# Optimization experiments

Measured on AMD Instinct MI355X. Metric: run time of the kernel, lower is better.

## Reference

```python
import jax, jax.numpy as jnp
import numpy as np

B, N, C_IN, C_EMB, G = 16, 1024, 16, 64, 128
NEG = -1e12


def _lap(m):
    # m @ D^-1/2, transpose, @ D^-1/2  (matches torch code incl. transpose)
    d = jnp.sum(m, axis=1) ** -0.5
    return (m * d[None, :]).T * d[None, :]


def setup_inputs():
    key = jax.random.key(0)
    ks = jax.random.split(key, 16)
    f = jax.random.normal
    return {
        'x': f(ks[0], (B, C_IN, N), jnp.float32),
        'ct': f(ks[1], (B, C_EMB, N), jnp.float32),
        'graph_data': jax.random.uniform(ks[2], (2, N, N), dtype=jnp.float32),
        'emb_w': f(ks[3], (C_EMB, C_IN)) / np.sqrt(C_IN).astype(np.float32),
        'emb_b': f(ks[4], (C_EMB,)) * 0.01,
        'emb2_w': f(ks[5], (N, N)) / np.sqrt(N).astype(np.float32),
        'emb2_b': f(ks[6], (N,)) * 0.01,
        'att_W': f(ks[7], (C_EMB, C_EMB)) / np.sqrt(C_EMB).astype(np.float32),
        'att_a': f(ks[8], (2 * C_EMB, 1)) / np.sqrt(2 * C_EMB).astype(np.float32),
        'att_GL': f(ks[9], (N, G)) / np.sqrt(G).astype(np.float32),
        'uai_w': f(ks[10], (C_EMB, C_EMB)) / np.sqrt(C_EMB).astype(np.float32),
        'uai_b': f(ks[11], (C_EMB,)) * 0.01,
        'lin1_w': f(ks[12], (C_EMB, C_EMB)) / np.sqrt(C_EMB).astype(np.float32),
        'lin2_w': f(ks[13], (C_EMB, C_EMB)) / np.sqrt(C_EMB).astype(np.float32),
        'lin2_b': f(ks[14], (C_EMB,)) * 0.01,
        'ln_w': jnp.ones((C_EMB, N), jnp.float32),
        'ln_b': jnp.zeros((C_EMB, N), jnp.float32),
    }


def reference(x, ct, graph_data, emb_w, emb_b, emb2_w, emb2_b, att_W, att_a,
              att_GL, uai_w, uai_b, lin1_w, lin2_w, lin2_b, ln_w, ln_b):
    # emb: Conv1d k=1 -> leaky_relu -> Linear over node axis N
    h0 = jax.nn.leaky_relu(jnp.einsum('bcn,ec->ben', x, emb_w) + emb_b[None, :, None])
    h0 = jnp.einsum('ben,mn->bem', h0, emb2_w) + emb2_b[None, None, :]
    inp = jnp.swapaxes(h0, 1, 2)  # [B,N,C']

    # InterpositionAttention (repeat/cat factorized: e_ij = leakyrelu(a1.h_i + a2.h_j))
    eye = jnp.eye(N, dtype=x.dtype)
    adj_att = jax.nn.softmax(jax.nn.relu(att_GL @ att_GL.T), axis=-1) + eye
    h = inp @ att_W  # [B,N,C']
    e = jax.nn.leaky_relu((h @ att_a[:C_EMB]) + jnp.swapaxes(h @ att_a[C_EMB:], 1, 2))  # [B,N,N]
    att = jax.nn.softmax(jnp.where(adj_att > 0, e, NEG), axis=2)
    x_att = jnp.swapaxes(jax.nn.relu(att @ h), 1, 2)  # [B,C',N]

    # UAI module (eval mode: dropout off -> all MC samples equal -> sigma = 0)
    mu = jnp.swapaxes(x_att, 1, 2) @ uai_w.T + uai_b  # [B,N,C']
    x_uai = jnp.swapaxes(mu, 1, 2)  # [B,C',N]

    g1 = _lap(graph_data[0] + eye)
    g2 = _lap(graph_data[1] + eye)

    # learned adjacency from pairwise squared distances (cdist p=2, squared)
    xf = jnp.swapaxes(x_uai, 1, 2)  # [B,N,C']
    sq = jnp.sum(xf * xf, axis=-1)
    d2 = jnp.maximum(sq[:, :, None] + sq[:, None, :] - 2.0 * (xf @ jnp.swapaxes(xf, 1, 2)), 0.0)
    gl = jax.nn.softmax(jnp.exp(-d2 / (2.0 * C_EMB)) + eye, axis=-1)  # sigma^2 = emb_size

    def ln(z):  # LayerNorm over last two dims [C', N]
        m = jnp.mean(z, axis=(1, 2), keepdims=True)
        v = jnp.var(z, axis=(1, 2), keepdims=True)
        return (z - m) / jnp.sqrt(v + 1e-5) * ln_w + ln_b

    l1 = lambda z: jnp.einsum('oc,bcn->bon', lin1_w, z)
    l2 = lambda z: jnp.einsum('oc,bcn->bon', lin2_w, z) + lin2_b[None, :, None]

    x_new = ln(l1(x_uai) @ gl + l1(l1(x_uai) @ g1) @ g2)
    ft = jax.nn.gelu(ln(l2(x_uai) @ gl + l2(l2(x_uai) @ g1) @ g2), approximate=False)
    rt = ft  # rt is computed by the identical expression (dropout off)

    ct_new = ft * ct + x_new - ft * x_new
    ht = rt * jax.nn.elu(ct_new) + x_uai - rt * x_uai
    return (ht, ct_new)
```

## Files before the change

### kernel.cpp

```cpp
#include <hip/hip_runtime.h>
#include <math.h>

typedef unsigned short u16;
typedef __attribute__((ext_vector_type(8))) short short8;
typedef __attribute__((ext_vector_type(4))) float floatx4;

constexpr int BATCH = 16;
constexpr int NI = 1024;
constexpr int CE = 64;
constexpr int CI = 16;
constexpr long long NN2  = (long long)NI * NI;
constexpr long long BCN  = (long long)BATCH * CE * NI;
constexpr long long BNv  = (long long)BATCH * NI;
constexpr long long BNN  = (long long)BATCH * NI * NI;
constexpr long long S1 = (long long)CE * NI;
constexpr long long S2 = 2 * S1;
constexpr int ZERON = (int)(2 * BNv + 80);

__device__ __forceinline__ float lrelu01(float x) { return x > 0.f ? x : 0.01f * x; }

__device__ __forceinline__ u16 f2bf(float f) {
  unsigned u = __builtin_bit_cast(unsigned, f);
  return (u16)((u + 0x7fffu + ((u >> 16) & 1u)) >> 16);
}
__device__ __forceinline__ float bf2f(u16 h) {
  unsigned u = ((unsigned)h) << 16;
  return __builtin_bit_cast(float, u);
}
__device__ __forceinline__ unsigned fkey(float f) {
  unsigned u = __builtin_bit_cast(unsigned, f);
  return (u & 0x80000000u) ? ~u : (u | 0x80000000u);
}
__device__ __forceinline__ float funkey(unsigned k) {
  unsigned u = (k & 0x80000000u) ? (k & 0x7fffffffu) : ~k;
  return __builtin_bit_cast(float, u);
}

__device__ __forceinline__ void gload16(const u16* g, u16* l) {
  __builtin_amdgcn_global_load_lds(
      (const __attribute__((address_space(1))) void*)g,
      (__attribute__((address_space(3))) void*)l, 16, 0, 0);
}

__device__ __forceinline__ void fence13() {
  __builtin_amdgcn_sched_barrier(0);
  asm volatile("s_waitcnt vmcnt(2) lgkmcnt(0)" ::: "memory");
  __builtin_amdgcn_s_barrier();
  __builtin_amdgcn_sched_barrier(0);
}

template<int N>
__device__ __forceinline__ void fence_bar() {
  __builtin_amdgcn_sched_barrier(0);
  if constexpr (N == 0) asm volatile("s_waitcnt vmcnt(0)" ::: "memory");
  else if constexpr (N == 1) asm volatile("s_waitcnt vmcnt(1)" ::: "memory");
  else if constexpr (N == 2) asm volatile("s_waitcnt vmcnt(2)" ::: "memory");
  else if constexpr (N == 3) asm volatile("s_waitcnt vmcnt(3)" ::: "memory");
  else if constexpr (N == 4) asm volatile("s_waitcnt vmcnt(4)" ::: "memory");
  else if constexpr (N == 6) asm volatile("s_waitcnt vmcnt(6)" ::: "memory");
  else asm volatile("s_waitcnt vmcnt(0)" ::: "memory");
  __builtin_amdgcn_s_barrier();
  __builtin_amdgcn_sched_barrier(0);
}

template<int BM, int BN, int MODE>
__global__ __launch_bounds__(256) void mgemm(
    const u16* __restrict__ Ag, const u16* __restrict__ B1g, const u16* __restrict__ B2g,
    int K1, int K, int lda, int ldb, long long bsA, long long bsB1,
    float* __restrict__ Cf, u16* __restrict__ Cb, int ldc, long long bsC,
    const float* __restrict__ aux1, const float* __restrict__ aux2,
    const float* __restrict__ aux3, const float* __restrict__ aux4,
    float* __restrict__ Zout)
{
  constexpr int RM = BM / 2, RN = BN / 2, MI = RM / 16, NJ = RN / 16;
  constexpr bool PIPE3 = (MODE == 14 || MODE == 15);
  constexpr int NBB = PIPE3 ? 3 : (MODE == 13 ? 3 : 1);
  constexpr int NBA = PIPE3 ? 3 : (MODE == 13 ? 2 : 1);
  constexpr int NLA = (BM * 8) / 256;
  constexpr int NLB = (BN * 8) / 256;
  constexpr int L = (NLA + NLB);
  constexpr int ASZ = (MODE == 5) ? 3 * BM * 128 : NBA * BM * 64;
  constexpr int BSZ = (MODE == 5) ? 3 * BN * 128 : NBB * BN * 64;
  __shared__ __align__(16) u16 As[ASZ];
  __shared__ __align__(16) u16 Bs[BSZ];
  __shared__ __align__(16) u16 xa[MODE == 13 ? 32 * 72 : 1];
  const int tid = threadIdx.x;
  int z, n0, r0, job15 = 0;
  bool job4 = false;
  long long cboff = 0;
  if constexpr (MODE == 15) {
    const int id = blockIdx.x;
    if (id >= 512 && id < 1536) {
      const int m = id - 512;
      float s = 0.f, sv = 0.f;
      for (int n = tid; n < NI; n += 256) {
        float g = aux3[(long long)m * NI + n] * aux2[n];
        s += g;
        sv = fmaf(g, aux1[n], sv);
      }
      float* r1 = (float*)As;
      float* r2 = (float*)As + 256;
      r1[tid] = s; r2[tid] = sv; __syncthreads();
      for (int st = 128; st > 0; st >>= 1) {
        if (tid < st) { r1[tid] += r1[tid + st]; r2[tid] += r2[tid + st]; }
        __syncthreads();
      }
      if (tid == 0) {
        float dm = aux2[m];
        Cf[m] = dm * (r1[0] + dm);
        Zout[m] = dm * (r2[0] + dm * aux1[m]);
      }
      return;
    }
    if (id >= 1536) {
      const int id2 = id - 1536;
      job15 = 2;
      z = id2 >> 5; r0 = (id2 & 1) * BM; n0 = ((id2 >> 1) & 15) * BN;
    } else {
      z = 0; n0 = (id & 15) * BN; r0 = (id >> 4) * BM;
    }
  } else if constexpr (MODE == 5) {
    const int fid = blockIdx.x;
    const int xcd = fid & 7, idx = fid >> 3;
    const int idx2 = idx >> 5;
    z = xcd + (idx2 >> 1) * 8;
    r0 = (idx2 & 1) * BM;
    n0 = (idx & 31) * BN;
  } else if constexpr (MODE == 3) {
    const int id = blockIdx.x;
    if (id < 4096) {
      const int xcd = id & 7, idx = id >> 3;
      z = (idx >> 8) * 8 + xcd;
      const int g = idx & 255;
      n0 = (g & 15) * 64; r0 = ((g >> 4) & 15) * 64;
    } else {
      const int t4 = id - 4096;
      job4 = true;
      z = t4 >> 6;
      const int g = t4 & 63;
      r0 = (g >> 4) * 64;
      n0 = (g & 15) * 64;
    }
  } else if constexpr (MODE == 13 || MODE == 14) {
    const int id = blockIdx.x;
    const int xcd = id & 7, idx = id >> 3;
    z = (idx >> 5) * 8 + xcd;
    if constexpr (MODE == 13) { r0 = (idx & 31) * BM; n0 = 0; }
    else { n0 = (idx & 31) * BN; r0 = 0; }
  } else {
    z = blockIdx.z; n0 = blockIdx.x * BN; r0 = blockIdx.y * BM;
  }
  int Kv = K, K1v = K1, ldav = lda, ldbv = ldb;
  const u16 *Ab, *Bb1;
  if constexpr (MODE == 15) {
    if (job15 == 2) {
      Kv = 64; K1v = 128; ldav = 64; ldbv = 64;
      Ab = B2g + (long long)r0 * 64;
      Bb1 = (const u16*)aux4 + (long long)z * S1 + (long long)n0 * 64;
      cboff = bsB1 + (long long)z * S1;
    } else {
      Ab = Ag + (long long)r0 * lda;
      Bb1 = B1g + (long long)n0 * ldb;
    }
  } else {
    Ab = Ag + (long long)z * bsA + (long long)r0 * ldav;
    Bb1 = B1g + (long long)z * bsB1 + (long long)n0 * ldbv;
    if constexpr (MODE == 3) {
      if (job4) Ab = ((const u16*)aux2) + (long long)r0 * 64;
    }
  }
  const int lane = tid & 63;
  const int wid = tid >> 6;
  const int wr = wid >> 1, wc = wid & 1;
  const int q = lane >> 4, mlow = lane & 15;
  const int wbase = tid & ~63;

  floatx4 acc[MI][NJ] = {};
  float zp0 = 0.f;

  float s1r_13 = 0.f, mr_13 = 0.f;
  const float* s2z_13 = nullptr;
  float4 sa, sb;
  if constexpr (MODE == 13) {
    const float* s1z = aux2 + (long long)z * NI;
    s2z_13 = aux3 + (long long)z * NI;
    const float mb = funkey(((const unsigned*)aux4)[z]);
    s1r_13 = s1z[r0 + (tid >> 3)];
    mr_13 = lrelu01(s1r_13 + mb);
  }

  auto stageAB = [&](int buf, int k0) {
    if constexpr (MODE != 13) {
      const u16* Asrc = Ab + k0;
#pragma unroll
      for (int s = 0; s < NLA; s++) {
        int cid = tid + s * 256;
        int r = cid >> 3, cc = cid & 7;
        gload16(Asrc + (long long)r * ldav + ((cc ^ (r & 7)) << 3),
                As + buf * (BM * 64) + ((wbase + s * 256) << 3));
      }
    }
    const u16* Bsrc = (k0 < K1v) ? (Bb1 + k0)
                                 : (B2g + (long long)n0 * ldbv + (k0 - K1v));
#pragma unroll
    for (int s = 0; s < NLB; s++) {
      int cid = tid + s * 256;
      int r = cid >> 3, cc = cid & 7;
      gload16(Bsrc + (long long)r * ldbv + ((cc ^ (r & 7)) << 3),
              Bs + buf * (BN * 64) + ((wbase + s * 256) << 3));
    }
  };

  auto agen_ld = [&](int k0) {
    const float* sp = s2z_13 + k0 + (tid & 7) * 8;
    sa = *(const float4*)sp;
    sb = *(const float4*)(sp + 4);
  };
  auto agen_st = [&](int buf) {
    int r = tid >> 3, craw = tid & 7;
    float p0 = __expf(lrelu01(s1r_13 + sa.x) - mr_13);
    float p1 = __expf(lrelu01(s1r_13 + sa.y) - mr_13);
    float p2 = __expf(lrelu01(s1r_13 + sa.z) - mr_13);
    float p3 = __expf(lrelu01(s1r_13 + sa.w) - mr_13);
    float p4 = __expf(lrelu01(s1r_13 + sb.x) - mr_13);
    float p5 = __expf(lrelu01(s1r_13 + sb.y) - mr_13);
    float p6 = __expf(lrelu01(s1r_13 + sb.z) - mr_13);
    float p7 = __expf(lrelu01(s1r_13 + sb.w) - mr_13);
    zp0 += p0 + p1 + p2 + p3 + p4 + p5 + p6 + p7;
    uint4 v;
    v.x = (unsigned)f2bf(p0) | ((unsigned)f2bf(p1) << 16);
    v.y = (unsigned)f2bf(p2) | ((unsigned)f2bf(p3) << 16);
    v.z = (unsigned)f2bf(p4) | ((unsigned)f2bf(p5) << 16);
    v.w = (unsigned)f2bf(p6) | ((unsigned)f2bf(p7) << 16);
    *(uint4*)&As[buf * (BM * 64) + (r * 8 + (craw ^ (r & 7))) * 8] = v;
  };

  auto compute_tile = [&](int bufA, int bufB) {
#pragma unroll
    for (int kh = 0; kh < 2; kh++) {
      const int kc = kh * 4 + q;
      short8 afr[MI], bfr[NJ];
#pragma unroll
      for (int i = 0; i < MI; i++) {
        int row = wr * RM + i * 16 + mlow;
        afr[i] = *(const short8*)&As[bufA * (BM * 64) + (row * 8 + (kc ^ (row & 7))) * 8];
      }
#pragma unroll
      for (int j = 0; j < NJ; j++) {
        int row = wc * RN + j * 16 + mlow;
        bfr[j] = *(const short8*)&Bs[bufB * (BN * 64) + (row * 8 + (kc ^ (row & 7))) * 8];
      }
#pragma unroll
      for (int i = 0; i < MI; i++)
#pragma unroll
        for (int j = 0; j < NJ; j++)
          acc[i][j] = __builtin_amdgcn_mfma_f32_16x16x32_bf16(afr[i], bfr[j], acc[i][j], 0, 0, 0);
    }
  };

  if constexpr (PIPE3) {
    const int nk = Kv >> 6;
#pragma unroll
    for (int p = 0; p < 2; p++) {
      int kk = (p < nk) ? p : (nk - 1);
      stageAB(p, kk << 6);
    }
    fence_bar<L>();
    int cur = 0, stg = 2;
    for (int ki = 0; ki < nk; ki++) {
      if (ki + 2 < nk) stageAB(stg, (ki + 2) << 6);
      compute_tile(cur, cur);
      if (ki + 1 < nk) {
        const int rem = nk - 1 - ki;
        const int u = (rem < 2) ? rem : 2;
        if (u == 2) fence_bar<L>();
        else fence_bar<0>();
      }
      cur++; if (cur == NBB) cur = 0;
      stg++; if (stg == NBB) stg = 0;
    }
    __syncthreads();
  } else if constexpr (MODE == 5) {
    const int ns = Kv >> 7;
    auto stage5 = [&](int buf, int s) {
#pragma unroll
      for (int sub = 0; sub < 2; sub++) {
        const int k0 = (s << 7) + (sub << 6);
        const u16* Asrc = Ab + k0;
#pragma unroll
        for (int g = 0; g < NLA; g++) {
          int cid = tid + g * 256;
          int r = cid >> 3, cc = cid & 7;
          gload16(Asrc + (long long)r * ldav + ((cc ^ (r & 7)) << 3),
                  As + buf * (BM * 128) + sub * (BM * 64) + ((wbase + g * 256) << 3));
        }
        const u16* Bsrc = (k0 < K1v) ? (Bb1 + k0)
                                     : (B2g + (long long)n0 * ldbv + (k0 - K1v));
#pragma unroll
        for (int g = 0; g < NLB; g++) {
          int cid = tid + g * 256;
          int r = cid >> 3, cc = cid & 7;
          gload16(Bsrc + (long long)r * ldbv + ((cc ^ (r & 7)) << 3),
                  Bs + buf * (BN * 128) + sub * (BN * 64) + ((wbase + g * 256) << 3));
        }
      }
    };
    auto compute5 = [&](int buf) {
#pragma unroll
      for (int sub = 0; sub < 2; sub++) {
#pragma unroll
        for (int kh = 0; kh < 2; kh++) {
          const int kc = kh * 4 + q;
          short8 afr[MI], bfr[NJ];
#pragma unroll
          for (int i = 0; i < MI; i++) {
            int row = wr * RM + i * 16 + mlow;
            afr[i] = *(const short8*)&As[buf * (BM * 128) + sub * (BM * 64) +
                                         (row * 8 + (kc ^ (row & 7))) * 8];
          }
#pragma unroll
          for (int j = 0; j < NJ; j++) {
            int row = wc * RN + j * 16 + mlow;
            bfr[j] = *(const short8*)&Bs[buf * (BN * 128) + sub * (BN * 64) +
                                         (row * 8 + (kc ^ (row & 7))) * 8];
          }
#pragma unroll
          for (int i = 0; i < MI; i++)
#pragma unroll
            for (int j = 0; j < NJ; j++)
              acc[i][j] = __builtin_amdgcn_mfma_f32_16x16x32_bf16(afr[i], bfr[j], acc[i][j], 0, 0, 0);
        }
      }
    };
    stage5(0, 0);
    stage5(1, 1);
    fence_bar<6>();
    for (int ki = 0; ki < ns; ki++) {
      if (ki + 2 < ns) stage5((ki + 2) % 3, ki + 2);
      compute5(ki % 3);
      if (ki + 1 < ns) {
        const int rem = ns - 1 - ki;
        if (rem >= 2) fence_bar<6>();
        else fence_bar<0>();
      }
    }
    __syncthreads();
  } else if constexpr (MODE == 13) {
    const int nk = Kv >> 6;
    agen_ld(0);
    stageAB(0, 0);
    if (nk > 1) stageAB(1, 64);
    agen_st(0);
    fence13();
    for (int ki = 0; ki < nk; ki++) {
      if (ki + 1 < nk) agen_ld((ki + 1) << 6);
      if (ki + 2 < nk) stageAB((ki + 2) % 3, (ki + 2) << 6);
      if (ki + 1 < nk) agen_st((ki + 1) & 1);
      compute_tile(ki & 1, ki % 3);
      fence13();
    }
  } else {
    for (int k0 = 0; k0 < Kv; k0 += 64) {
      stageAB(0, k0);
      __syncthreads();
      compute_tile(0, 0);
      __syncthreads();
    }
  }

  if constexpr (MODE == 3) {
    if (job4) {
      u16* abig = (u16*)Cf;
#pragma unroll
      for (int i = 0; i < MI; i++) {
#pragma unroll
        for (int j = 0; j < NJ; j++) {
#pragma unroll
          for (int rg = 0; rg < 4; rg++) {
            int r = r0 + wr * RM + i * 16 + q * 4 + rg;
            int ncol = n0 + wc * RN + j * 16 + mlow;
            int blk = r >> 6, oo = r & 63;
            int drow = ((blk & 1) << 6) + oo;
            float v = acc[i][j][rg];
            if (blk < 2) v += aux3[drow];
            abig[(long long)z * (128 * 2048LL) + (long long)drow * 2048 +
                 (long long)(blk >> 1) * 1024 + ncol] = f2bf(v);
          }
        }
      }
    } else {
      const float* sqb = aux1 + (long long)z * NI;
#pragma unroll
      for (int i = 0; i < MI; i++) {
#pragma unroll
        for (int rg = 0; rg < 4; rg++) {
          int r = r0 + wr * RM + i * 16 + q * 4 + rg;
          float sqi = sqb[r];
          float rsum = 0.f;
#pragma unroll
          for (int j = 0; j < NJ; j++) {
            int ncol = n0 + wc * RN + j * 16 + mlow;
            float d2 = fmaxf(sqi + sqb[ncol] - 2.f * acc[i][j][rg], 0.f);
            float w = __expf(__expf(-d2 * (1.f / 128.f)) + (r == ncol ? 1.f : 0.f) - 2.f);
            Cb[(long long)z * bsC + (long long)r * ldc + ncol] = f2bf(w);
            rsum += w;
          }
          rsum += __shfl_xor(rsum, 1);
          rsum += __shfl_xor(rsum, 2);
          rsum += __shfl_xor(rsum, 4);
          rsum += __shfl_xor(rsum, 8);
          if (mlow == 0) atomicAdd(&Zout[(long long)z * NI + r], rsum);
        }
      }
    }
  } else if constexpr (MODE == 14) {
    float ps1 = 0.f, ps2 = 0.f;
#pragma unroll
    for (int i = 0; i < MI; i++) {
#pragma unroll
      for (int rg = 0; rg < 4; rg++) {
        int r = wr * RM + i * 16 + q * 4 + rg;
        int ncol = n0 + wc * RN + mlow;
        float v = acc[i][0][rg] + aux3[r] * aux1[ncol];
        Cb[(long long)z * bsC + (long long)r * ldc + ncol] = f2bf(v);
        ps1 = fmaf(v, aux2[r], ps1);
        ps2 = fmaf(v, aux2[64 + r], ps2);
      }
    }
    ps1 += __shfl_xor(ps1, 16); ps1 += __shfl_xor(ps1, 32);
    ps2 += __shfl_xor(ps2, 16); ps2 += __shfl_xor(ps2, 32);
    float* sred = (float*)As;
    const int col = wc * RN + mlow;
    if (q == 0) { sred[col * 2 + wr] = ps1; sred[64 + col * 2 + wr] = ps2; }
    __syncthreads();
    if (tid < 32) {
      float v1 = sred[tid * 2] + sred[tid * 2 + 1];
      float v2 = sred[64 + tid * 2] + sred[64 + tid * 2 + 1];
      Cf[(long long)z * NI + n0 + tid] = v1;
      Zout[(long long)z * NI + n0 + tid] = v2;
      float mx = v2;
      for (int off = 1; off < 32; off <<= 1) mx = fmaxf(mx, __shfl_xor(mx, off));
      if (tid == 0) atomicMax((unsigned*)B2g + z, fkey(mx));
    }
  } else if constexpr (MODE == 13) {
    float* zred = (float*)xa;
    float* zinv = (float*)xa + 256;
    zred[(tid >> 3) * 8 + (tid & 7)] = zp0;
    __syncthreads();
    if (tid < 32) {
      float sum = 0.f;
#pragma unroll
      for (int j = 0; j < 8; j++) sum += zred[tid * 8 + j];
      zinv[tid] = 1.f / sum;
    }
    __syncthreads();
    float zr[4];
#pragma unroll
    for (int rg = 0; rg < 4; rg++) zr[rg] = zinv[wr * 16 + q * 4 + rg];
    __syncthreads();
#pragma unroll
    for (int j = 0; j < NJ; j++) {
#pragma unroll
      for (int rg = 0; rg < 4; rg++) {
        int row = wr * 16 + q * 4 + rg;
        int col = wc * RN + j * 16 + mlow;
        float v = fmaxf(acc[0][j][rg] * zr[rg], 0.f);
        xa[row * 72 + col] = f2bf(v);
      }
    }
#pragma unroll
    for (int s = 0; s < 2; s++) {
      int cid = tid + s * 256;
      int r = cid >> 3, cc = cid & 7;
      gload16(B2g + r * 64 + ((cc ^ (r & 7)) << 3),
              Bs + ((wbase + s * 256) << 3));
    }
    __syncthreads();
    floatx4 acc2[2] = {};
#pragma unroll
    for (int kh = 0; kh < 2; kh++) {
      const int kc = kh * 4 + q;
      short8 a2 = *(const short8*)&xa[(wr * 16 + mlow) * 72 + kc * 8];
#pragma unroll
      for (int j = 0; j < 2; j++) {
        int orow = wc * 32 + j * 16 + mlow;
        short8 b2 = *(const short8*)&Bs[(orow * 8 + (kc ^ (orow & 7))) * 8];
        acc2[j] = __builtin_amdgcn_mfma_f32_16x16x32_bf16(a2, b2, acc2[j], 0, 0, 0);
      }
    }
#pragma unroll
    for (int rg = 0; rg < 4; rg++) {
      int row = r0 + wr * 16 + q * 4 + rg;
      float sqp = 0.f;
#pragma unroll
      for (int j = 0; j < 2; j++) {
        int o = wc * 32 + j * 16 + mlow;
        float v = acc2[j][rg] + aux1[o];
        Cb[(long long)z * bsC + (long long)row * ldc + o] = f2bf(v);
        sqp = fmaf(v, v, sqp);
      }
      sqp += __shfl_xor(sqp, 1);
      sqp += __shfl_xor(sqp, 2);
      sqp += __shfl_xor(sqp, 4);
      sqp += __shfl_xor(sqp, 8);
      if (mlow == 0) atomicAdd(&Zout[(long long)z * NI + row], sqp);
    }
  } else if constexpr (MODE == 5) {
    float ts = 0.f, tss = 0.f;
#pragma unroll
    for (int i = 0; i < MI; i++) {
#pragma unroll
      for (int j = 0; j < NJ; j++) {
#pragma unroll
        for (int rg = 0; rg < 4; rg++) {
          int r = r0 + wr * RM + i * 16 + q * 4 + rg;
          int ncol = n0 + wc * RN + j * 16 + mlow;
          float v = acc[i][j][rg];
          v += aux3[r] * aux1[ncol] + aux4[r] * aux2[ncol];
          Cb[(long long)z * bsC + (long long)r * ldc + ncol] = f2bf(v);
          ts += v;
          tss = fmaf(v, v, tss);
        }
      }
    }
    float* red = (float*)As;
    red[tid] = ts; red[256 + tid] = tss;
    __syncthreads();
    for (int st = 128; st > 0; st >>= 1) {
      if (tid < st) { red[tid] += red[tid + st]; red[256 + tid] += red[256 + tid + st]; }
      __syncthreads();
    }
    if (tid == 0) {
      const int half = r0 >> 6;
      atomicAdd(&Zout[z * 2 + half], red[0]);
      atomicAdd(&Zout[32 + z * 2 + half], red[256]);
    }
  } else {
#pragma unroll
    for (int i = 0; i < MI; i++) {
#pragma unroll
      for (int j = 0; j < NJ; j++) {
#pragma unroll
        for (int rg = 0; rg < 4; rg++) {
          int r = r0 + wr * RM + i * 16 + q * 4 + rg;
          int ncol = n0 + wc * RN + j * 16 + mlow;
          Cb[cboff + (long long)r * ldc + ncol] = f2bf(acc[i][j][rg]);
        }
      }
    }
  }
}

__global__ __launch_bounds__(256) void adiv(u16* __restrict__ abig,
                                            const float* __restrict__ Zgl)
{
  const int bid = blockIdx.x;
  const int z = bid >> 6;
  const int r = (bid & 63) * 2;
  const int t = threadIdx.x;
  const int c = t * 4;
  const float4 zv = *(const float4*)(Zgl + (long long)z * NI + c);
  const float i0 = __builtin_amdgcn_rcpf(zv.x);
  const float i1 = __builtin_amdgcn_rcpf(zv.y);
  const float i2 = __builtin_amdgcn_rcpf(zv.z);
  const float i3 = __builtin_amdgcn_rcpf(zv.w);
  u16* base = abig + (long long)z * (128 * 2048LL) + (long long)r * 2048 + c;
#pragma unroll
  for (int rr = 0; rr < 2; rr++) {
    u16* p = base + (long long)rr * 2048;
    uint2 v = *(uint2*)p;
    u16 o[4];
    o[0] = f2bf(bf2f((u16)(v.x & 0xffff)) * i0);
    o[1] = f2bf(bf2f((u16)(v.x >> 16)) * i1);
    o[2] = f2bf(bf2f((u16)(v.y & 0xffff)) * i2);
    o[3] = f2bf(bf2f((u16)(v.y >> 16)) * i3);
    *(uint2*)p = *(uint2*)o;
  }
}

__global__ __launch_bounds__(256) void lap_rowsum(const float* __restrict__ gd,
                                                  float* __restrict__ dr,
                                                  float* __restrict__ zero)
{
  if (blockIdx.x >= 2048) {
    int i = (blockIdx.x - 2048) * 256 + threadIdx.x;
    if (i < ZERON) zero[i] = 0.f;
    return;
  }
  const int ki = blockIdx.x;
  const float* row = gd + (long long)ki * NI;
  float s = 0.f;
  for (int j = threadIdx.x; j < NI; j += 256) s += row[j];
  __shared__ float red[256];
  red[threadIdx.x] = s; __syncthreads();
  for (int st = 128; st > 0; st >>= 1) {
    if (threadIdx.x < st) red[threadIdx.x] += red[threadIdx.x + st];
    __syncthreads();
  }
  if (threadIdx.x == 0) dr[ki] = rsqrtf(red[0] + 1.f);
}

__global__ __launch_bounds__(256) void mega_prep(
    const float* __restrict__ l1w, const float* __restrict__ l2w,
    const float* __restrict__ l2b, const float* __restrict__ uaiw,
    const float* __restrict__ attW,
    u16* __restrict__ stack4, float* __restrict__ rb2ext, float* __restrict__ rl2ext,
    u16* __restrict__ uaiw_bf, u16* __restrict__ attwT_bf, float* __restrict__ wcs,
    const float* __restrict__ emb2w, u16* __restrict__ emb2w_bf,
    const float* __restrict__ x, const float* __restrict__ ew,
    const float* __restrict__ eb, u16* __restrict__ h0aT,
    const float* __restrict__ gd, const float* __restrict__ dsum,
    u16* __restrict__ g2t, u16* __restrict__ g1,
    float* __restrict__ cs1)
{
  __shared__ float sm[1092];
  const int bid = blockIdx.x;
  const int t = threadIdx.x;
  if (bid < 98) {
    const int gid = bid * 256 + t;
    if (gid < 4096) {
      stack4[gid] = f2bf(l1w[gid]);
    } else if (gid < 8192) {
      stack4[gid] = f2bf(l2w[gid - 4096]);
    } else if (gid < 12288) {
      int tt = gid - 8192, o = tt >> 6, m = tt & 63;
      float s = 0.f;
      for (int c = 0; c < 64; c++) s = fmaf(l1w[o * 64 + c], l1w[c * 64 + m], s);
      stack4[gid] = f2bf(s);
    } else if (gid < 16384) {
      int tt = gid - 12288, o = tt >> 6, m = tt & 63;
      float s = 0.f;
      for (int c = 0; c < 64; c++) s = fmaf(l2w[o * 64 + c], l2w[c * 64 + m], s);
      stack4[gid] = f2bf(s);
    } else if (gid < 16512) {
      int r = gid - 16384;
      rb2ext[r] = (r < 64) ? 0.f : l2b[r - 64];
    } else if (gid < 16640) {
      int r = gid - 16512;
      float v = 0.f;
      if (r >= 64) { int o = r - 64; for (int c = 0; c < 64; c++) v = fmaf(l2w[o * 64 + c], l2b[c], v); }
      rl2ext[r] = v;
    } else if (gid < 20736) {
      uaiw_bf[gid - 16640] = f2bf(uaiw[gid - 16640]);
    } else if (gid < 24832) {
      int idx = gid - 20736;
      int c = idx >> 6, e = idx & 63;
      attwT_bf[idx] = f2bf(attW[e * 64 + c]);
    } else if (gid < 24896) {
      int c = gid - 24832;
      float s = 0.f;
      for (int e = 0; e < 64; e++) s += attW[e * 64 + c];
      wcs[c] = s;
    }
  } else if (bid < 1122) {
    const long long i = (long long)(bid - 98) * 1024 + t * 4;
    float4 v = *(const float4*)(emb2w + i);
    u16 o4[4] = {f2bf(v.x), f2bf(v.y), f2bf(v.z), f2bf(v.w)};
    *(uint2*)(emb2w_bf + i) = *(const uint2*)o4;
  } else if (bid < 1378) {
    const int sub = bid - 1122;
    const int b = sub >> 4;
    const int nc = (sub & 15) * 64;
    float* we = sm;
    float* be = sm + 1024;
    for (int i = t; i < 1024; i += 256) we[i] = ew[i];
    if (t < 64) be[t] = eb[t];
    __syncthreads();
    const int n = nc + (t >> 2);
    const int e0 = (t & 3) * 16;
    const float* xb = x + (long long)b * CI * NI + n;
    float xv[16];
#pragma unroll
    for (int c = 0; c < CI; c++) xv[c] = xb[(long long)c * NI];
    u16 out16[16];
#pragma unroll
    for (int ee = 0; ee < 16; ee++) {
      const int e = e0 + ee;
      float a = be[e];
#pragma unroll
      for (int c = 0; c < CI; c++) a = fmaf(xv[c], we[e * 16 + c], a);
      out16[ee] = f2bf(lrelu01(a));
    }
    u16* dst = h0aT + (long long)b * S1 + (long long)n * 64 + e0;
    *(uint4*)dst = *(uint4*)out16;
    *(uint4*)(dst + 8) = *(uint4*)(out16 + 8);
  } else if (bid < 2402) {
    const int m = bid - 1378;
    const int j = t * 4;
    const float* d = dsum + NI;
    float4 g = *(const float4*)(gd + NN2 + (long long)m * NI + j);
    float dm = d[m];
    float4 dj = *(const float4*)(d + j);
    u16 o4[4];
    o4[0] = f2bf((g.x + (m == j     ? 1.f : 0.f)) * dm * dj.x);
    o4[1] = f2bf((g.y + (m == j + 1 ? 1.f : 0.f)) * dm * dj.y);
    o4[2] = f2bf((g.z + (m == j + 2 ? 1.f : 0.f)) * dm * dj.z);
    o4[3] = f2bf((g.w + (m == j + 3 ? 1.f : 0.f)) * dm * dj.w);
    *(uint2*)(g2t + (long long)m * NI + j) = *(const uint2*)o4;
  } else if (bid < 3426) {
    const int sub = bid - 2402;
    const int bx = (sub & 31) * 32, by = (sub >> 5) * 32;
    const int lx = t & 31, ly = t >> 5;
    float* tile = sm;
    for (int yy = ly; yy < 32; yy += 8)
      tile[yy * 33 + lx] = gd[(long long)(by + yy) * NI + bx + lx];
    __syncthreads();
    for (int yy = ly; yy < 32; yy += 8) {
      const int i = bx + yy, j = by + lx;
      float v = (tile[lx * 33 + yy] + (i == j ? 1.f : 0.f)) * dsum[i] * dsum[j];
      g1[(long long)i * NI + j] = f2bf(v);
    }
  } else {
    const int n = bid - 3426;
    float s = 0.f;
    for (int i = t; i < NI; i += 256) s = fmaf(gd[(long long)n * NI + i], dsum[i], s);
    float* red = sm;
    red[t] = s; __syncthreads();
    for (int st = 128; st > 0; st >>= 1) {
      if (t < st) red[t] += red[t + st];
      __syncthreads();
    }
    if (t == 0) cs1[n] = dsum[n] * (red[0] + dsum[n]);
  }
}

__global__ __launch_bounds__(512) void ln_final_t(const u16* __restrict__ T,
                                                  const float* __restrict__ stats,
                                                  const float* __restrict__ lnw,
                                                  const float* __restrict__ lnb,
                                                  const float* __restrict__ ct,
                                                  const u16* __restrict__ xuT,
                                                  float* __restrict__ outp)
{
  __shared__ float xs[64 * 65];
  const int blk = blockIdx.x;
  const int b = blk >> 4;
  const int n0 = (blk & 15) << 6;
  const int t = threadIdx.x;
  const int tc = t & 63, tr = t >> 6;
#pragma unroll
  for (int i = 0; i < 8; i++) {
    int nn = i * 8 + tr;
    xs[tc * 65 + nn] = bf2f(xuT[((long long)b << 16) + (long long)(n0 + nn) * 64 + tc]);
  }
  __syncthreads();
  const float inv_n = 1.f / 65536.f;
  const float m0 = stats[b * 2] * inv_n;
  const float m1 = stats[b * 2 + 1] * inv_n;
  const float rs0 = rsqrtf(fmaxf(stats[32 + b * 2] * inv_n - m0 * m0, 0.f) + 1e-5f);
  const float rs1 = rsqrtf(fmaxf(stats[32 + b * 2 + 1] * inv_n - m1 * m1, 0.f) + 1e-5f);
#pragma unroll
  for (int j = 0; j < 8; j++) {
    const int c = j * 8 + tr;
    const int n = n0 + tc;
    const int rem = c * NI + n;
    const long long toff = (long long)b * S2 + rem;
    const float t0 = bf2f(T[toff]);
    const float t1 = bf2f(T[toff + S1]);
    const float w = lnw[rem], bb = lnb[rem];
    const float xn = (t0 - m0) * rs0 * w + bb;
    float ft = (t1 - m1) * rs1 * w + bb;
    ft = 0.5f * ft * (1.f + erff(ft * 0.70710678118654752f));
    const float u = xs[c * 65 + tc];
    const long long oidx = ((long long)b << 16) + rem;
    const float cn = fmaf(ft, ct[oidx] - xn, xn);
    const float el = cn > 0.f ? cn : expm1f(cn);
    outp[oidx] = fmaf(ft, el - u, u);
    outp[BCN + oidx] = cn;
  }
}

extern "C" void kernel_launch(void* const* d_in, const int* in_sizes, int n_in,
                              void* d_out, int out_size, void* d_ws, size_t ws_size,
                              hipStream_t stream)
{
  (void)in_sizes; (void)n_in; (void)out_size; (void)ws_size;
  const float* x      = (const float*)d_in[0];
  const float* ct     = (const float*)d_in[1];
  const float* gdata  = (const float*)d_in[2];
  const float* emb_w  = (const float*)d_in[3];
  const float* emb_b  = (const float*)d_in[4];
  const float* emb2_w = (const float*)d_in[5];
  const float* emb2_b = (const float*)d_in[6];
  const float* att_W  = (const float*)d_in[7];
  const float* att_a  = (const float*)d_in[8];
  const float* uai_w  = (const float*)d_in[10];
  const float* uai_b  = (const float*)d_in[11];
  const float* lin1_w = (const float*)d_in[12];
  const float* lin2_w = (const float*)d_in[13];
  const float* lin2_b = (const float*)d_in[14];
  const float* ln_w   = (const float*)d_in[15];
  const float* ln_b   = (const float*)d_in[16];
  float* outp = (float*)d_out;

  float* ws = (float*)d_ws;
  long long o = 0;
  auto af = [&](long long n) { float* p = ws + o; o += (n + 63) & ~63LL; return p; };
  auto au = [&](long long n) { return (u16*)af((n + 1) / 2); };

  float* s1      = af(BNv);
  float* s2      = af(BNv);
  float* dsum    = af(2 * NI);
  float* cs1v    = af(NI);
  float* cs2v    = af(NI);
  float* v2v     = af(NI);
  float* rb2ext  = af(128);
  float* rl2ext  = af(128);
  float* wcs     = af(64);
  float* zeroreg = af(ZERON);
  float* Zgl     = zeroreg;
  float* sqv     = zeroreg + BNv;
  float* stats   = zeroreg + 2 * BNv;
  unsigned* s2mU = (unsigned*)(stats + 64);
  u16* Tacc      = au(S2 * BATCH);
  u16* emb2w_bf  = au(NN2);
  u16* h0aTb     = au(S1 * BATCH);
  u16* ybf       = au(S1 * BATCH);
  u16* hTb       = au(S1 * BATCH);
  u16* xuaiTb    = au(S1 * BATCH);
  u16* g1b       = au(NN2);
  u16* g2tb      = au(NN2);
  u16* G12b      = au(NN2);
  u16* Abig      = au((long long)BATCH * 128 * 2048);
  u16* stack4    = au(256 * 64);
  u16* uaiw_bf   = au(CE * CE);
  u16* attwT_bf  = au(CE * CE);
  u16* bigW      = au(BNN);

  lap_rowsum<<<2048 + (ZERON + 255) / 256, 256, 0, stream>>>(gdata, dsum, zeroreg);

  mega_prep<<<4450, 256, 0, stream>>>(
      lin1_w, lin2_w, lin2_b, uai_w, att_W,
      stack4, rb2ext, rl2ext, uaiw_bf, attwT_bf, wcs,
      emb2_w, emb2w_bf, x, emb_w, emb_b, h0aTb,
      gdata, dsum, g2tb, g1b, cs1v);

  mgemm<32, 64, 15><<<2048, 256, 0, stream>>>(
      g2tb, g1b, attwT_bf, NI, NI, NI, NI, 0, (long long)(ybf - G12b),
      cs2v, G12b, NI, 0, cs1v, dsum + NI, gdata + NN2, (const float*)h0aTb, v2v);

  mgemm<64, 32, 14><<<512, 256, 0, stream>>>(
      ybf, emb2w_bf, (const u16*)s2mU, NI, NI, NI, NI, S1, 0,
      s1, hTb, NI, S1, emb2_b, att_a, wcs, nullptr, s2);

  mgemm<32, 64, 13><<<512, 256, 0, stream>>>(
      hTb, hTb, uaiw_bf, NI, NI, NI, NI, 0, S1,
      nullptr, xuaiTb, CE, S1, uai_b, s1, s2, (const float*)s2mU, sqv);

  mgemm<64, 64, 3><<<5120, 256, 0, stream>>>(
      xuaiTb, xuaiTb, nullptr, CE, CE, CE, CE, S1, S1,
      (float*)Abig, bigW, NI, NN2, sqv, (const float*)stack4, rb2ext, nullptr, Zgl);

  adiv<<<1024, 256, 0, stream>>>(Abig, Zgl);

  mgemm<64, 32, 5><<<1024, 256, 0, stream>>>(
      Abig, bigW, G12b, NI, 2 * NI, 2048, NI, (long long)128 * 2048, NN2,
      nullptr, Tacc, NI, S2, cs2v, v2v, rb2ext, rl2ext, stats);

  ln_final_t<<<256, 512, 0, stream>>>(Tacc, stats, ln_w, ln_b, ct, xuaiTb, outp);
}
```

Baseline: 225.3 us.

## Enlarge MODE 5 GEMM tile to 128x64 and reuse shared 3-stage pipeline

Switches the final fused GEMM (MODE 5) from 64x32 tiles with a custom 128-deep K staging loop to 128x64 tiles that cover both row halves, and routes it through the generic 3-buffer PIPE3 pipeline. Block mapping changes so each block handles the full 128 rows of a batch slice, with the LayerNorm partial-sum reduction split into two 128-thread halves that feed the two stats slots. This raises operand reuse per loaded tile and cuts redundant loads of the B operand. The cost is 4x fewer blocks (256), which may leave compute units underfilled, plus more registers per thread.

```diff
diff --git a/kernel.cpp b/kernel.cpp
--- a/kernel.cpp
+++ b/kernel.cpp
@@ -73,16 +73,14 @@
     float* __restrict__ Zout)
 {
   constexpr int RM = BM / 2, RN = BN / 2, MI = RM / 16, NJ = RN / 16;
-  constexpr bool PIPE3 = (MODE == 14 || MODE == 15);
+  constexpr bool PIPE3 = (MODE == 5 || MODE == 14 || MODE == 15);
   constexpr int NBB = PIPE3 ? 3 : (MODE == 13 ? 3 : 1);
   constexpr int NBA = PIPE3 ? 3 : (MODE == 13 ? 2 : 1);
   constexpr int NLA = (BM * 8) / 256;
   constexpr int NLB = (BN * 8) / 256;
   constexpr int L = (NLA + NLB);
-  constexpr int ASZ = (MODE == 5) ? 3 * BM * 128 : NBA * BM * 64;
-  constexpr int BSZ = (MODE == 5) ? 3 * BN * 128 : NBB * BN * 64;
-  __shared__ __align__(16) u16 As[ASZ];
-  __shared__ __align__(16) u16 Bs[BSZ];
+  __shared__ __align__(16) u16 As[NBA * BM * 64];
+  __shared__ __align__(16) u16 Bs[NBB * BN * 64];
   __shared__ __align__(16) u16 xa[MODE == 13 ? 32 * 72 : 1];
   const int tid = threadIdx.x;
   int z, n0, r0, job15 = 0;
@@ -120,12 +118,11 @@
       z = 0; n0 = (id & 15) * BN; r0 = (id >> 4) * BM;
     }
   } else if constexpr (MODE == 5) {
-    const int fid = blockIdx.x;
-    const int xcd = fid & 7, idx = fid >> 3;
-    const int idx2 = idx >> 5;
-    z = xcd + (idx2 >> 1) * 8;
-    r0 = (idx2 & 1) * BM;
-    n0 = (idx & 31) * BN;
+    const int id = blockIdx.x;
+    const int xcd = id & 7, idx = id >> 3;
+    z = (idx & 1) * 8 + xcd;
+    r0 = 0;
+    n0 = (idx >> 1) * BN;
   } else if constexpr (MODE == 3) {
     const int id = blockIdx.x;
     if (id < 4096) {
@@ -280,71 +277,6 @@
       stg++; if (stg == NBB) stg = 0;
     }
     __syncthreads();
-  } else if constexpr (MODE == 5) {
-    const int ns = Kv >> 7;
-    auto stage5 = [&](int buf, int s) {
-#pragma unroll
-      for (int sub = 0; sub < 2; sub++) {
-        const int k0 = (s << 7) + (sub << 6);
-        const u16* Asrc = Ab + k0;
-#pragma unroll
-        for (int g = 0; g < NLA; g++) {
-          int cid = tid + g * 256;
-          int r = cid >> 3, cc = cid & 7;
-          gload16(Asrc + (long long)r * ldav + ((cc ^ (r & 7)) << 3),
-                  As + buf * (BM * 128) + sub * (BM * 64) + ((wbase + g * 256) << 3));
-        }
-        const u16* Bsrc = (k0 < K1v) ? (Bb1 + k0)
-                                     : (B2g + (long long)n0 * ldbv + (k0 - K1v));
-#pragma unroll
-        for (int g = 0; g < NLB; g++) {
-          int cid = tid + g * 256;
-          int r = cid >> 3, cc = cid & 7;
-          gload16(Bsrc + (long long)r * ldbv + ((cc ^ (r & 7)) << 3),
-                  Bs + buf * (BN * 128) + sub * (BN * 64) + ((wbase + g * 256) << 3));
-        }
-      }
-    };
-    auto compute5 = [&](int buf) {
-#pragma unroll
-      for (int sub = 0; sub < 2; sub++) {
-#pragma unroll
-        for (int kh = 0; kh < 2; kh++) {
-          const int kc = kh * 4 + q;
-          short8 afr[MI], bfr[NJ];
-#pragma unroll
-          for (int i = 0; i < MI; i++) {
-            int row = wr * RM + i * 16 + mlow;
-            afr[i] = *(const short8*)&As[buf * (BM * 128) + sub * (BM * 64) +
-                                         (row * 8 + (kc ^ (row & 7))) * 8];
-          }
-#pragma unroll
-          for (int j = 0; j < NJ; j++) {
-            int row = wc * RN + j * 16 + mlow;
-            bfr[j] = *(const short8*)&Bs[buf * (BN * 128) + sub * (BN * 64) +
-                                         (row * 8 + (kc ^ (row & 7))) * 8];
-          }
-#pragma unroll
-          for (int i = 0; i < MI; i++)
-#pragma unroll
-            for (int j = 0; j < NJ; j++)
-              acc[i][j] = __builtin_amdgcn_mfma_f32_16x16x32_bf16(afr[i], bfr[j], acc[i][j], 0, 0, 0);
-        }
-      }
-    };
-    stage5(0, 0);
-    stage5(1, 1);
-    fence_bar<6>();
-    for (int ki = 0; ki < ns; ki++) {
-      if (ki + 2 < ns) stage5((ki + 2) % 3, ki + 2);
-      compute5(ki % 3);
-      if (ki + 1 < ns) {
-        const int rem = ns - 1 - ki;
-        if (rem >= 2) fence_bar<6>();
-        else fence_bar<0>();
-      }
-    }
-    __syncthreads();
   } else if constexpr (MODE == 13) {
     const int nk = Kv >> 6;
     agen_ld(0);
@@ -513,7 +445,7 @@
       for (int j = 0; j < NJ; j++) {
 #pragma unroll
         for (int rg = 0; rg < 4; rg++) {
-          int r = r0 + wr * RM + i * 16 + q * 4 + rg;
+          int r = wr * RM + i * 16 + q * 4 + rg;
           int ncol = n0 + wc * RN + j * 16 + mlow;
           float v = acc[i][j][rg];
           v += aux3[r] * aux1[ncol] + aux4[r] * aux2[ncol];
@@ -526,14 +458,20 @@
     float* red = (float*)As;
     red[tid] = ts; red[256 + tid] = tss;
     __syncthreads();
-    for (int st = 128; st > 0; st >>= 1) {
-      if (tid < st) { red[tid] += red[tid + st]; red[256 + tid] += red[256 + tid + st]; }
+    for (int st = 64; st > 0; st >>= 1) {
+      if ((tid & 127) < st) {
+        red[tid] += red[tid + st];
+        red[256 + tid] += red[256 + tid + st];
+      }
       __syncthreads();
     }
     if (tid == 0) {
-      const int half = r0 >> 6;
-      atomicAdd(&Zout[z * 2 + half], red[0]);
-      atomicAdd(&Zout[32 + z * 2 + half], red[256]);
+      atomicAdd(&Zout[z * 2 + 0], red[0]);
+      atomicAdd(&Zout[32 + z * 2 + 0], red[256]);
+    }
+    if (tid == 128) {
+      atomicAdd(&Zout[z * 2 + 1], red[128]);
+      atomicAdd(&Zout[32 + z * 2 + 1], red[256 + 128]);
     }
   } else {
 #pragma unroll
@@ -853,7 +791,7 @@
 
   adiv<<<1024, 256, 0, stream>>>(Abig, Zgl);
 
-  mgemm<64, 32, 5><<<1024, 256, 0, stream>>>(
+  mgemm<128, 64, 5><<<256, 256, 0, stream>>>(
       Abig, bigW, G12b, NI, 2 * NI, 2048, NI, (long long)128 * 2048, NN2,
       nullptr, Tacc, NI, S2, cs2v, v2v, rb2ext, rl2ext, stats);
 
```

Result: faster. 220.7 us, median of 2 (-2.1%).
